# Performance work log

Measured on AMD Instinct MI355X. Metric: run time of the kernel, lower is better.

Reference implementation:

```python
import jax, jax.numpy as jnp
import numpy as np

K = 5        # spline kernel_size per dim (dim=2 -> 25 weight slots)
N = 60000    # input nodes
E = 360000   # input edges
N1 = 30000   # nodes after first graclus/max_pool
E2 = 180000  # edges of pooled graph
N2 = 15000   # nodes after second graclus pooling
G = 60       # graphs in batch


def _spline_basis(pseudo):
    """Open B-spline basis, degree 1, dim 2. pseudo: [E,2] in [0,1].
    Returns flat weight indices [E,4] and basis products [E,4]."""
    v = pseudo * (K - 1)
    i0 = jnp.clip(jnp.floor(v).astype(jnp.int32), 0, K - 1)   # [E,2]
    frac = v - jnp.floor(v)                                   # [E,2]
    idxs, ws = [], []
    for s0 in (0, 1):
        for s1 in (0, 1):
            ix = jnp.clip(i0[:, 0] + s0, 0, K - 1)
            iy = jnp.clip(i0[:, 1] + s1, 0, K - 1)
            w0 = frac[:, 0] if s0 else 1.0 - frac[:, 0]
            w1 = frac[:, 1] if s1 else 1.0 - frac[:, 1]
            idxs.append(ix + K * iy)
            ws.append(w0 * w1)
    return jnp.stack(idxs, -1), jnp.stack(ws, -1)


def _spline_conv(x, edge_index, pseudo, W, root, bias, num_nodes):
    """SplineConv: B-spline weighted messages, mean aggregation, root weight + bias."""
    src, dst = edge_index[0], edge_index[1]
    e = src.shape[0]
    idx, b = _spline_basis(pseudo)
    # dense per-edge basis over 25 kernel slots (only 4 nonzero per edge)
    B = jnp.zeros((e, K * K), x.dtype).at[jnp.arange(e)[:, None], idx].add(b)
    x_j = x[src]                                   # [E,Fin]
    fin, fout = W.shape[1], W.shape[2]
    xb = B[:, :, None] * x_j[:, None, :]           # [E,25,Fin]
    msg = xb.reshape(e, K * K * fin) @ W.reshape(K * K * fin, fout)
    agg = jax.ops.segment_sum(msg, dst, num_segments=num_nodes)
    cnt = jax.ops.segment_sum(jnp.ones((e,), x.dtype), dst, num_segments=num_nodes)
    agg = agg / jnp.maximum(cnt, 1.0)[:, None]     # mean aggregation
    return agg + x @ root + bias


def _seg_max_f(x, seg, n):
    m = jax.ops.segment_max(x, seg, num_segments=n)
    cnt = jax.ops.segment_sum(jnp.ones(seg.shape, x.dtype), seg, num_segments=n)
    return jnp.where((cnt > 0)[:, None], m, 0.0)


def _seg_max_i(x, seg, n):
    m = jax.ops.segment_max(x, seg, num_segments=n)
    return jnp.maximum(m, 0)


def _cartesian(pos, edge_index):
    # T.Cartesian(cat=False): attr = (pos[col]-pos[row]) / (2*max|.|) + 0.5
    cart = pos[edge_index[1]] - pos[edge_index[0]]
    scale = jnp.maximum(jnp.max(jnp.abs(cart)), 1e-12)
    return cart / (2.0 * scale) + 0.5


def setup_inputs():
    key = jax.random.key(0)
    ks = jax.random.split(key, 18)
    return {
        'x': jax.random.normal(ks[0], (N, 1), jnp.float32),
        'pos': jax.random.uniform(ks[1], (N, 2), jnp.float32),
        'edge_attr': jax.random.uniform(ks[2], (E, 2), jnp.float32),
        'edge_index': jax.random.randint(ks[3], (2, E), 0, N, jnp.int32),
        'batch': jnp.sort(jax.random.randint(ks[4], (N,), 0, G, jnp.int32)),
        'cluster1': jax.random.randint(ks[5], (N,), 0, N1, jnp.int32),
        'edge_index2': jax.random.randint(ks[6], (2, E2), 0, N1, jnp.int32),
        'cluster2': jax.random.randint(ks[7], (N1,), 0, N2, jnp.int32),
        'W1': jax.random.normal(ks[8], (K * K, 1, 32), jnp.float32) * 0.1,
        'root1': jax.random.normal(ks[9], (1, 32), jnp.float32) * 0.1,
        'bias1': jnp.zeros((32,), jnp.float32),
        'W2': jax.random.normal(ks[10], (K * K, 32, 64), jnp.float32) * 0.05,
        'root2': jax.random.normal(ks[11], (32, 64), jnp.float32) * 0.05,
        'bias2': jnp.zeros((64,), jnp.float32),
        'fc1_w': jax.random.normal(ks[12], (64, 128), jnp.float32) * 0.05,
        'fc1_b': jnp.zeros((128,), jnp.float32),
        'fc2_w': jax.random.normal(ks[13], (128, 3), jnp.float32) * 0.05,
        'fc2_b': jnp.zeros((3,), jnp.float32),
    }


def reference(x, pos, edge_attr, edge_index, batch, cluster1, edge_index2,
              cluster2, W1, root1, bias1, W2, root2, bias2,
              fc1_w, fc1_b, fc2_w, fc2_b):
    # conv1 + elu
    h = jax.nn.elu(_spline_conv(x, edge_index, edge_attr, W1, root1, bias1, N))
    # max_pool over graclus cluster1 (cluster given as input), Cartesian edge attrs
    x1 = _seg_max_f(h, cluster1, N1)
    pcnt = jax.ops.segment_sum(jnp.ones((N,), pos.dtype), cluster1, num_segments=N1)
    pos1 = jax.ops.segment_sum(pos, cluster1, num_segments=N1) / jnp.maximum(pcnt, 1.0)[:, None]
    batch1 = _seg_max_i(batch, cluster1, N1)
    attr2 = _cartesian(pos1, edge_index2)
    # conv2 + elu
    h2 = jax.nn.elu(_spline_conv(x1, edge_index2, attr2, W2, root2, bias2, N1))
    # max_pool_x over cluster2
    x2 = _seg_max_f(h2, cluster2, N2)
    batch2 = _seg_max_i(batch1, cluster2, N2)
    # global mean pool over graphs
    gsum = jax.ops.segment_sum(x2, batch2, num_segments=G)
    gcnt = jax.ops.segment_sum(jnp.ones((N2,), x2.dtype), batch2, num_segments=G)
    gm = gsum / jnp.maximum(gcnt, 1.0)[:, None]
    # head (dropout is identity in eval mode)
    h3 = jax.nn.elu(gm @ fc1_w + fc1_b)
    logits = h3 @ fc2_w + fc2_b
    return jax.nn.log_softmax(logits, axis=1)
```

## Files before the change

### kernel.cpp

```cpp
#include <hip/hip_runtime.h>
#include <math.h>

#define KD 5
#define NN 60000
#define EE 360000
#define NP1 30000
#define EE2 180000
#define NP2 15000
#define GG 60

#define FH 16
#define NBLK 512

#define PB2 120
#define CPB2 125


__device__ __forceinline__ unsigned fkey(float f) {
    unsigned u = __float_as_uint(f);
    return (u & 0x80000000u) ? ~u : (u | 0x80000000u);
}
__device__ __forceinline__ float fkey_inv(unsigned k) {
    unsigned u = (k & 0x80000000u) ? (k ^ 0x80000000u) : ~k;
    return __uint_as_float(u);
}

__device__ __forceinline__ void spline_basis(float p0, float p1, int* idx, float* w) {
    float v0 = p0 * 4.0f, v1 = p1 * 4.0f;
    float fl0 = floorf(v0), fl1 = floorf(v1);
    int i0 = min(max((int)fl0, 0), KD - 1);
    int i1 = min(max((int)fl1, 0), KD - 1);
    float fr0 = v0 - fl0, fr1 = v1 - fl1;
    int c = 0;
#pragma unroll
    for (int s0 = 0; s0 < 2; ++s0) {
#pragma unroll
        for (int s1 = 0; s1 < 2; ++s1) {
            int ix = min(i0 + s0, KD - 1);
            int iy = min(i1 + s1, KD - 1);
            float w0 = s0 ? fr0 : 1.0f - fr0;
            float w1 = s1 ? fr1 : 1.0f - fr1;
            idx[c] = ix + KD * iy;
            w[c] = w0 * w1;
            ++c;
        }
    }
}

__device__ __forceinline__ float elu1(float v) {
    return v > 0.0f ? v : expm1f(v);
}


__global__ void conv1_edge(const float* __restrict__ x, const float* __restrict__ ea,
                           const int* __restrict__ ei, const float* __restrict__ W1,
                           float* __restrict__ agg1, float* __restrict__ cnt1) {
    int gid = blockIdx.x * blockDim.x + threadIdx.x;
    if (gid >= EE * 32) return;
    int e = gid >> 5, f = gid & 31;
    int src = ei[e], dst = ei[EE + e];
    int idx[4]; float w[4];
    spline_basis(ea[2 * e], ea[2 * e + 1], idx, w);
    float coeff = 0.0f;
#pragma unroll
    for (int k = 0; k < 4; ++k) coeff += w[k] * W1[idx[k] * 32 + f];
    atomicAdd(&agg1[dst * 32 + f], x[src] * coeff);
    if (f == 0) atomicAdd(&cnt1[dst], 1.0f);
}


__global__ void conv1fin_pool1(const float* __restrict__ x, const float* __restrict__ root1,
                               const float* __restrict__ bias1, const float* __restrict__ cnt1,
                               const float* __restrict__ agg1, const float* __restrict__ pos,
                               const int* __restrict__ batch, const int* __restrict__ cl1,
                               unsigned* __restrict__ x1key, int* __restrict__ ccnt1,
                               float* __restrict__ pos1, int* __restrict__ batch1) {
    int gid = blockIdx.x * blockDim.x + threadIdx.x;
    if (gid >= NN * 32) return;
    int n = gid >> 5, f = gid & 31;
    float v = elu1(agg1[gid] / fmaxf(cnt1[n], 1.0f) + x[n] * root1[f] + bias1[f]);
    int c = cl1[n];
    atomicMax(&x1key[c * 32 + f], fkey(v));
    if (f == 0) {
        atomicAdd(&ccnt1[c], 1);
        atomicAdd(&pos1[c * 2], pos[n * 2]);
        atomicAdd(&pos1[c * 2 + 1], pos[n * 2 + 1]);
        atomicMax(&batch1[c], batch[n]);
    }
}

__global__ void pool1_fin(unsigned* __restrict__ x1key, const int* __restrict__ ccnt1,
                          float* __restrict__ pos1) {
    int gid = blockIdx.x * blockDim.x + threadIdx.x;
    if (gid >= NP1 * 32) return;
    int c = gid >> 5, f = gid & 31;
    int cnt = ccnt1[c];
    float v = cnt > 0 ? fkey_inv(x1key[gid]) : 0.0f;
    ((float*)x1key)[gid] = v;
    if (f < 2) pos1[c * 2 + f] = pos1[c * 2 + f] / fmaxf((float)cnt, 1.0f);
}


__global__ void cart_k(const float* __restrict__ pos1, const int* __restrict__ ei2,
                       float* __restrict__ attr2, unsigned* __restrict__ scaleb) {
    int e = blockIdx.x * blockDim.x + threadIdx.x;
    float m = 0.0f;
    if (e < EE2) {
        int s = ei2[e], d = ei2[EE2 + e];
        float c0 = pos1[d * 2] - pos1[s * 2];
        float c1 = pos1[d * 2 + 1] - pos1[s * 2 + 1];
        attr2[e * 2] = c0;
        attr2[e * 2 + 1] = c1;
        m = fmaxf(fabsf(c0), fabsf(c1));
    }
#pragma unroll
    for (int off = 32; off > 0; off >>= 1) m = fmaxf(m, __shfl_down(m, off));
    if ((threadIdx.x & 63) == 0) atomicMax(scaleb, __float_as_uint(m));
}

__global__ void attr2_fin(float* __restrict__ attr2, const unsigned* __restrict__ scaleb) {
    int gid = blockIdx.x * blockDim.x + threadIdx.x;
    if (gid >= EE2 * 2) return;
    float s = fmaxf(__uint_as_float(*scaleb), 1e-12f);
    attr2[gid] = attr2[gid] / (2.0f * s) + 0.5f;
}


__global__ __launch_bounds__(256) void conv2_lds(const float* __restrict__ x1,
                                                 const float* __restrict__ attr2,
                                                 const int* __restrict__ ei2,
                                                 const float* __restrict__ W2,
                                                 float* __restrict__ agg2,
                                                 float* __restrict__ cnt2) {
    __shared__ float wl[25 * 8 * FH * 4];
    const int q = blockIdx.x & 3;
    const int blk = blockIdx.x >> 2;
    const int t = threadIdx.x;

    for (int i = t; i < 25 * 8 * FH * 4; i += 256) {
        int c = i & 3;
        int fh = (i >> 2) & (FH - 1);
        int g = (i >> 6) & 7;
        int s = i >> 9;
        wl[i] = W2[s * 2048 + (g * 4 + c) * 64 + q * FH + fh];
    }
    __syncthreads();

    const int fh = t & (FH - 1);
    const int grp = t >> 4;
    const int EPB = (EE2 + NBLK - 1) / NBLK;
    const int e0 = blk * EPB;
    const int e_end = min(e0 + EPB, EE2);
    const float4* wl4 = (const float4*)wl;

    for (int e = e0 + grp; e < e_end; e += 16) {
        int src = ei2[e], dst = ei2[EE2 + e];
        int idx[4]; float w[4];
        spline_basis(attr2[2 * e], attr2[2 * e + 1], idx, w);
        const float4* xp = (const float4*)(x1 + src * 32);
        float4 xv[8];
#pragma unroll
        for (int g = 0; g < 8; ++g) xv[g] = xp[g];
        float msg = 0.0f;
#pragma unroll
        for (int k = 0; k < 4; ++k) {
            const float4* wp = wl4 + idx[k] * (8 * FH) + fh;
            float acc = 0.0f;
#pragma unroll
            for (int g = 0; g < 8; ++g) {
                float4 wv = wp[g * FH];
                acc += xv[g].x * wv.x;
                acc += xv[g].y * wv.y;
                acc += xv[g].z * wv.z;
                acc += xv[g].w * wv.w;
            }
            msg += w[k] * acc;
        }
        atomicAdd(&agg2[dst * 64 + q * FH + fh], msg);
        if (q == 0 && fh == 0) atomicAdd(&cnt2[dst], 1.0f);
    }
}


__global__ void conv2fin_pool2(const float* __restrict__ x1, const float* __restrict__ root2,
                               const float* __restrict__ bias2, const float* __restrict__ cnt2,
                               const float* __restrict__ agg2, const int* __restrict__ cl2,
                               const int* __restrict__ batch1, unsigned* __restrict__ x2key,
                               int* __restrict__ ccnt2, int* __restrict__ batch2) {
    int gid = blockIdx.x * blockDim.x + threadIdx.x;
    if (gid >= NP1 * 64) return;
    int n = gid >> 6, f = gid & 63;
    float r = 0.0f;
    const float* xs = x1 + n * 32;
#pragma unroll
    for (int i = 0; i < 32; ++i) r += xs[i] * root2[i * 64 + f];
    float v = elu1(agg2[gid] / fmaxf(cnt2[n], 1.0f) + r + bias2[f]);
    int c = cl2[n];
    atomicMax(&x2key[c * 64 + f], fkey(v));
    if (f == 0) {
        atomicAdd(&ccnt2[c], 1);
        atomicMax(&batch2[c], batch1[n]);
    }
}


__global__ __launch_bounds__(256) void pool2_part(const unsigned* __restrict__ x2key,
                                                  const int* __restrict__ ccnt2,
                                                  const int* __restrict__ batch2,
                                                  float* __restrict__ partial,
                                                  float* __restrict__ pcnt) {
    __shared__ float gs[GG * 64 + GG];
    const int t = threadIdx.x;
    for (int i = t; i < GG * 64 + GG; i += 256) gs[i] = 0.0f;
    __syncthreads();
    const int lane = t & 63, wv = t >> 6;
    const int c0 = blockIdx.x * CPB2;
    const int c1 = min(c0 + CPB2, NP2);
    for (int c = c0 + wv; c < c1; c += 4) {
        int cnt = ccnt2[c];
        int g = batch2[c];
        float v = cnt > 0 ? fkey_inv(x2key[c * 64 + lane]) : 0.0f;
        atomicAdd(&gs[g * 64 + lane], v);
        if (lane == 0) atomicAdd(&gs[GG * 64 + g], 1.0f);
    }
    __syncthreads();
    float* pb = partial + (size_t)blockIdx.x * (GG * 64);
    for (int i = t; i < GG * 64; i += 256) pb[i] = gs[i];
    if (t < GG) pcnt[blockIdx.x * GG + t] = gs[GG * 64 + t];
}


__global__ __launch_bounds__(128) void gpool_head(const float* __restrict__ partial,
                                                  const float* __restrict__ pcnt,
                                                  const float* __restrict__ fc1w,
                                                  const float* __restrict__ fc1b,
                                                  const float* __restrict__ fc2w,
                                                  const float* __restrict__ fc2b,
                                                  float* __restrict__ out) {
    const int g = blockIdx.x;
    const int t = threadIdx.x;
    __shared__ float red[128];
    __shared__ float acc2[128];
    __shared__ float gm[64];
    __shared__ float h3[128];
    __shared__ float lg[3];

    red[t] = (t < PB2) ? pcnt[t * GG + g] : 0.0f;
    __syncthreads();
    for (int s = 64; s > 0; s >>= 1) {
        if (t < s) red[t] += red[t + s];
        __syncthreads();
    }

    const int f = t & 63, h = t >> 6;
    float acc = 0.0f;
    for (int b = h * (PB2 / 2); b < (h + 1) * (PB2 / 2); ++b)
        acc += partial[(size_t)b * (GG * 64) + g * 64 + f];
    acc2[t] = acc;
    __syncthreads();
    if (t < 64) gm[t] = (acc2[t] + acc2[t + 64]) / fmaxf(red[0], 1.0f);
    __syncthreads();

    float a = fc1b[t];
#pragma unroll
    for (int i = 0; i < 64; ++i) a += gm[i] * fc1w[i * 128 + t];
    h3[t] = elu1(a);
    __syncthreads();
    if (t < 3) {
        float a2 = fc2b[t];
#pragma unroll
        for (int i = 0; i < 128; ++i) a2 += h3[i] * fc2w[i * 3 + t];
        lg[t] = a2;
    }
    __syncthreads();
    if (t == 0) {
        float m = fmaxf(lg[0], fmaxf(lg[1], lg[2]));
        float s = expf(lg[0] - m) + expf(lg[1] - m) + expf(lg[2] - m);
        float lse = m + logf(s);
        out[g * 3 + 0] = lg[0] - lse;
        out[g * 3 + 1] = lg[1] - lse;
        out[g * 3 + 2] = lg[2] - lse;
    }
}


extern "C" void kernel_launch(void* const* d_in, const int* in_sizes, int n_in,
                              void* d_out, int out_size, void* d_ws, size_t ws_size,
                              hipStream_t stream) {
    const float* x     = (const float*)d_in[0];
    const float* pos   = (const float*)d_in[1];
    const float* eattr = (const float*)d_in[2];
    const int*   ei    = (const int*)d_in[3];
    const int*   batch = (const int*)d_in[4];
    const int*   cl1   = (const int*)d_in[5];
    const int*   ei2   = (const int*)d_in[6];
    const int*   cl2   = (const int*)d_in[7];
    const float* W1    = (const float*)d_in[8];
    const float* root1 = (const float*)d_in[9];
    const float* bias1 = (const float*)d_in[10];
    const float* W2    = (const float*)d_in[11];
    const float* root2 = (const float*)d_in[12];
    const float* bias2 = (const float*)d_in[13];
    const float* fc1w  = (const float*)d_in[14];
    const float* fc1b  = (const float*)d_in[15];
    const float* fc2w  = (const float*)d_in[16];
    const float* fc2b  = (const float*)d_in[17];
    float* out = (float*)d_out;

    char* p = (char*)d_ws;
    auto carve = [&](size_t bytes) {
        char* r = p;
        p += (bytes + 255) & ~(size_t)255;
        return r;
    };
    float*    agg1    = (float*)carve((size_t)NN * 32 * 4);
    float*    cnt1    = (float*)carve((size_t)NN * 4);
    unsigned* x1key   = (unsigned*)carve((size_t)NP1 * 32 * 4);
    int*      ccnt1   = (int*)carve((size_t)NP1 * 4);
    float*    pos1    = (float*)carve((size_t)NP1 * 2 * 4);
    int*      batch1  = (int*)carve((size_t)NP1 * 4);
    unsigned* scaleb  = (unsigned*)carve(4);
    float*    agg2    = (float*)carve((size_t)NP1 * 64 * 4);
    float*    cnt2    = (float*)carve((size_t)NP1 * 4);
    unsigned* x2key   = (unsigned*)carve((size_t)NP2 * 64 * 4);
    int*      ccnt2   = (int*)carve((size_t)NP2 * 4);
    int*      batch2  = (int*)carve((size_t)NP2 * 4);
    size_t zero_bytes = (size_t)(p - (char*)d_ws);
    float*    attr2   = (float*)carve((size_t)EE2 * 2 * 4);
    float*    partial = (float*)carve((size_t)PB2 * GG * 64 * 4);
    float*    pcnt    = (float*)carve((size_t)PB2 * GG * 4);

    hipMemsetAsync(d_ws, 0, zero_bytes, stream);

    const int B = 256;
    conv1_edge<<<(EE * 32 + B - 1) / B, B, 0, stream>>>(x, eattr, ei, W1, agg1, cnt1);
    conv1fin_pool1<<<(NN * 32 + B - 1) / B, B, 0, stream>>>(x, root1, bias1, cnt1, agg1,
                                                            pos, batch, cl1, x1key, ccnt1,
                                                            pos1, batch1);
    pool1_fin<<<(NP1 * 32 + B - 1) / B, B, 0, stream>>>(x1key, ccnt1, pos1);
    cart_k<<<(EE2 + B - 1) / B, B, 0, stream>>>(pos1, ei2, attr2, scaleb);
    attr2_fin<<<(EE2 * 2 + B - 1) / B, B, 0, stream>>>(attr2, scaleb);
    conv2_lds<<<NBLK * 4, B, 0, stream>>>((const float*)x1key, attr2, ei2, W2, agg2, cnt2);
    conv2fin_pool2<<<(NP1 * 64 + B - 1) / B, B, 0, stream>>>((const float*)x1key, root2, bias2,
                                                             cnt2, agg2, cl2, batch1, x2key,
                                                             ccnt2, batch2);
    pool2_part<<<PB2, B, 0, stream>>>(x2key, ccnt2, batch2, partial, pcnt);
    gpool_head<<<GG, 128, 0, stream>>>(partial, pcnt, fc1w, fc1b, fc2w, fc2b, out);
}
```

Before: 266.1 us.

## Use packed fp16 dot2 for conv2 messages and fold attr normalization into conv2

Conv2 now gathers pooled node features and spline weights as packed fp16 pairs and accumulates with the v_dot2 instruction. This halves the gather bandwidth and the LDS footprint and cuts the FMA count. The separate attr2 normalization kernel is removed, and the scaling is applied inside conv2 from the stored max. The trade-off is reduced precision in the conv2 inputs and weights, which is rounded toward zero to fp16.

```diff
diff --git a/kernel.cpp b/kernel.cpp
--- a/kernel.cpp
+++ b/kernel.cpp
@@ -14,6 +14,13 @@
 
 #define PB2 120
 #define CPB2 125
+
+typedef _Float16 h2 __attribute__((ext_vector_type(2)));
+
+__device__ __forceinline__ float dot2h(unsigned w, unsigned x, float c) {
+    return __builtin_amdgcn_fdot2(__builtin_bit_cast(h2, w),
+                                  __builtin_bit_cast(h2, x), c, false);
+}
 
 
 __device__ __forceinline__ unsigned fkey(float f) {
@@ -90,27 +97,31 @@
 }
 
 __global__ void pool1_fin(unsigned* __restrict__ x1key, const int* __restrict__ ccnt1,
-                          float* __restrict__ pos1) {
+                          float* __restrict__ pos1, unsigned* __restrict__ x1h) {
     int gid = blockIdx.x * blockDim.x + threadIdx.x;
     if (gid >= NP1 * 32) return;
     int c = gid >> 5, f = gid & 31;
     int cnt = ccnt1[c];
     float v = cnt > 0 ? fkey_inv(x1key[gid]) : 0.0f;
     ((float*)x1key)[gid] = v;
+    float vn = __shfl_xor(v, 1);
+    if ((f & 1) == 0)
+        x1h[c * 16 + (f >> 1)] = __builtin_bit_cast(unsigned,
+                                     __builtin_amdgcn_cvt_pkrtz(v, vn));
     if (f < 2) pos1[c * 2 + f] = pos1[c * 2 + f] / fmaxf((float)cnt, 1.0f);
 }
 
 
 __global__ void cart_k(const float* __restrict__ pos1, const int* __restrict__ ei2,
-                       float* __restrict__ attr2, unsigned* __restrict__ scaleb) {
+                       float* __restrict__ cart, unsigned* __restrict__ scaleb) {
     int e = blockIdx.x * blockDim.x + threadIdx.x;
     float m = 0.0f;
     if (e < EE2) {
         int s = ei2[e], d = ei2[EE2 + e];
         float c0 = pos1[d * 2] - pos1[s * 2];
         float c1 = pos1[d * 2 + 1] - pos1[s * 2 + 1];
-        attr2[e * 2] = c0;
-        attr2[e * 2 + 1] = c1;
+        cart[e * 2] = c0;
+        cart[e * 2 + 1] = c1;
         m = fmaxf(fabsf(c0), fabsf(c1));
     }
 #pragma unroll
@@ -118,61 +129,61 @@
     if ((threadIdx.x & 63) == 0) atomicMax(scaleb, __float_as_uint(m));
 }
 
-__global__ void attr2_fin(float* __restrict__ attr2, const unsigned* __restrict__ scaleb) {
-    int gid = blockIdx.x * blockDim.x + threadIdx.x;
-    if (gid >= EE2 * 2) return;
-    float s = fmaxf(__uint_as_float(*scaleb), 1e-12f);
-    attr2[gid] = attr2[gid] / (2.0f * s) + 0.5f;
-}
-
-
-__global__ __launch_bounds__(256) void conv2_lds(const float* __restrict__ x1,
-                                                 const float* __restrict__ attr2,
+
+__global__ __launch_bounds__(256) void conv2_f16(const unsigned* __restrict__ x1h,
+                                                 const float* __restrict__ cart,
                                                  const int* __restrict__ ei2,
+                                                 const unsigned* __restrict__ scaleb,
                                                  const float* __restrict__ W2,
                                                  float* __restrict__ agg2,
                                                  float* __restrict__ cnt2) {
-    __shared__ float wl[25 * 8 * FH * 4];
+    __shared__ unsigned wl[25 * 4 * 16 * 4];
     const int q = blockIdx.x & 3;
     const int blk = blockIdx.x >> 2;
     const int t = threadIdx.x;
 
-    for (int i = t; i < 25 * 8 * FH * 4; i += 256) {
-        int c = i & 3;
-        int fh = (i >> 2) & (FH - 1);
-        int g = (i >> 6) & 7;
-        int s = i >> 9;
-        wl[i] = W2[s * 2048 + (g * 4 + c) * 64 + q * FH + fh];
-    }
-    __syncthreads();
-
+    for (int i = t; i < 6400; i += 256) {
+        int pp = i & 3;
+        int fh = (i >> 2) & 15;
+        int gg = (i >> 6) & 3;
+        int s  = i >> 8;
+        int fi = gg * 8 + pp * 2;
+        int fo = q * FH + fh;
+        float w0 = W2[s * 2048 + fi * 64 + fo];
+        float w1 = W2[s * 2048 + (fi + 1) * 64 + fo];
+        wl[i] = __builtin_bit_cast(unsigned, __builtin_amdgcn_cvt_pkrtz(w0, w1));
+    }
+    __syncthreads();
+
+    const float sc = fmaxf(__uint_as_float(*scaleb), 1e-12f);
     const int fh = t & (FH - 1);
     const int grp = t >> 4;
     const int EPB = (EE2 + NBLK - 1) / NBLK;
     const int e0 = blk * EPB;
     const int e_end = min(e0 + EPB, EE2);
-    const float4* wl4 = (const float4*)wl;
+    const uint4* wl4 = (const uint4*)wl;
 
     for (int e = e0 + grp; e < e_end; e += 16) {
         int src = ei2[e], dst = ei2[EE2 + e];
+        float p0 = cart[2 * e] / (2.0f * sc) + 0.5f;
+        float p1 = cart[2 * e + 1] / (2.0f * sc) + 0.5f;
         int idx[4]; float w[4];
-        spline_basis(attr2[2 * e], attr2[2 * e + 1], idx, w);
-        const float4* xp = (const float4*)(x1 + src * 32);
-        float4 xv[8];
-#pragma unroll
-        for (int g = 0; g < 8; ++g) xv[g] = xp[g];
+        spline_basis(p0, p1, idx, w);
+        const uint4* xp = (const uint4*)(x1h + src * 16);
+        uint4 xq[4];
+#pragma unroll
+        for (int gg = 0; gg < 4; ++gg) xq[gg] = xp[gg];
         float msg = 0.0f;
 #pragma unroll
         for (int k = 0; k < 4; ++k) {
-            const float4* wp = wl4 + idx[k] * (8 * FH) + fh;
             float acc = 0.0f;
 #pragma unroll
-            for (int g = 0; g < 8; ++g) {
-                float4 wv = wp[g * FH];
-                acc += xv[g].x * wv.x;
-                acc += xv[g].y * wv.y;
-                acc += xv[g].z * wv.z;
-                acc += xv[g].w * wv.w;
+            for (int gg = 0; gg < 4; ++gg) {
+                uint4 wv = wl4[idx[k] * 64 + gg * 16 + fh];
+                acc = dot2h(wv.x, xq[gg].x, acc);
+                acc = dot2h(wv.y, xq[gg].y, acc);
+                acc = dot2h(wv.z, xq[gg].z, acc);
+                acc = dot2h(wv.w, xq[gg].w, acc);
             }
             msg += w[k] * acc;
         }
@@ -326,7 +337,8 @@
     int*      ccnt2   = (int*)carve((size_t)NP2 * 4);
     int*      batch2  = (int*)carve((size_t)NP2 * 4);
     size_t zero_bytes = (size_t)(p - (char*)d_ws);
-    float*    attr2   = (float*)carve((size_t)EE2 * 2 * 4);
+    unsigned* x1h     = (unsigned*)carve((size_t)NP1 * 16 * 4);
+    float*    cart    = (float*)carve((size_t)EE2 * 2 * 4);
     float*    partial = (float*)carve((size_t)PB2 * GG * 64 * 4);
     float*    pcnt    = (float*)carve((size_t)PB2 * GG * 4);
 
@@ -337,10 +349,9 @@
     conv1fin_pool1<<<(NN * 32 + B - 1) / B, B, 0, stream>>>(x, root1, bias1, cnt1, agg1,
                                                             pos, batch, cl1, x1key, ccnt1,
                                                             pos1, batch1);
-    pool1_fin<<<(NP1 * 32 + B - 1) / B, B, 0, stream>>>(x1key, ccnt1, pos1);
-    cart_k<<<(EE2 + B - 1) / B, B, 0, stream>>>(pos1, ei2, attr2, scaleb);
-    attr2_fin<<<(EE2 * 2 + B - 1) / B, B, 0, stream>>>(attr2, scaleb);
-    conv2_lds<<<NBLK * 4, B, 0, stream>>>((const float*)x1key, attr2, ei2, W2, agg2, cnt2);
+    pool1_fin<<<(NP1 * 32 + B - 1) / B, B, 0, stream>>>(x1key, ccnt1, pos1, x1h);
+    cart_k<<<(EE2 + B - 1) / B, B, 0, stream>>>(pos1, ei2, cart, scaleb);
+    conv2_f16<<<NBLK * 4, B, 0, stream>>>(x1h, cart, ei2, scaleb, W2, agg2, cnt2);
     conv2fin_pool2<<<(NP1 * 64 + B - 1) / B, B, 0, stream>>>((const float*)x1key, root2, bias2,
                                                              cnt2, agg2, cl2, batch1, x2key,
                                                              ccnt2, batch2);
```

Result: faster. 250.7 us (-5.8%).
